# Performance work log

Measured on AMD Instinct MI355X. Metric: run time of the kernel, lower is better.

## Reference

```python
import jax, jax.numpy as jnp
import numpy as np

EPS = 1e-4

def _softmax_kernel(data, projection_matrix, is_query):
    # data: [..., n, d], projection_matrix: [m, d]
    d = data.shape[-1]
    m = projection_matrix.shape[0]
    data_normalizer = 1.0 / (d ** 0.25)
    ratio = 1.0 / (m ** 0.5)
    # [..., n, m]
    data_dash = jnp.einsum('...id,jd->...ij', data_normalizer * data, projection_matrix)
    # ||x||^2 / 2 * normalizer^2, shape [..., n, 1]
    diag_data = (jnp.sum(data * data, axis=-1) * 0.5 * data_normalizer ** 2)[..., None]
    if is_query:
        stab = jnp.max(data_dash, axis=-1, keepdims=True)
    else:
        stab = jnp.max(data_dash)
    return ratio * (jnp.exp(data_dash - diag_data - stab) + EPS)

def _linear_attention(q, k, v):
    # q,k: [..., n, m] feature maps; v: [..., n, e]
    D_inv = 1.0 / jnp.einsum('...nd,...d->...n', q, k.sum(axis=-2))
    context = jnp.einsum('...nd,...ne->...de', k, v)  # [..., m, e]
    return jnp.einsum('...de,...nd,...n->...ne', context, q, D_inv)

def setup_inputs() -> dict:
    key = jax.random.key(0)
    k1, k2, k3, k4 = jax.random.split(key, 4)
    B, H, N, D, M = 8, 8, 4096, 64, 266
    return {
        'q': jax.random.normal(k1, (B, H, N, D), dtype=jnp.float32),
        'k': jax.random.normal(k2, (B, H, N, D), dtype=jnp.float32),
        'v': jax.random.normal(k3, (B, H, N, D), dtype=jnp.float32),
        'projection_matrix': jax.random.normal(k4, (M, D), dtype=jnp.float32),
    }

def reference(q, k, v, projection_matrix):
    q_prime = _softmax_kernel(q, projection_matrix, is_query=True)
    k_prime = _softmax_kernel(k, projection_matrix, is_query=False)
    return _linear_attention(q_prime, k_prime, v)
```

## Files before the change

kernel.cpp:

```cpp
#include <hip/hip_runtime.h>
#include <math.h>

#define BH    64
#define NSEQ  4096
#define DDIM  64
#define MDIM  266
#define MPAD  272
#define CSTR  288
#define KTS   40
#define QTS   296
#define RATIO 0.06131393394849658f
#define NORMF 0.35355339059327373f
#define DIAGF 0.0625f
#define EPSF  1e-4f

typedef __attribute__((ext_vector_type(8))) short bf16x8;
typedef __attribute__((ext_vector_type(4))) float f32x4;

__device__ __forceinline__ unsigned fenc(float f) {
  unsigned u = __float_as_uint(f);
  return (u & 0x80000000u) ? ~u : (u | 0x80000000u);
}
__device__ __forceinline__ float fdec(unsigned u) {
  return (u & 0x80000000u) ? __uint_as_float(u & 0x7fffffffu) : __uint_as_float(~u);
}

__device__ __forceinline__ void split1(float x, unsigned short& h, unsigned short& l) {
  unsigned ux = __float_as_uint(x);
  float hf = __uint_as_float(ux & 0xffff0000u);
  h = (unsigned short)(ux >> 16);
  l = (unsigned short)(__float_as_uint(x - hf) >> 16);
}

__device__ __forceinline__ void splitf(float4 a, float4 b, bf16x8& hi, bf16x8& lo) {
  float x[8] = {a.x, a.y, a.z, a.w, b.x, b.y, b.z, b.w};
#pragma unroll
  for (int e = 0; e < 8; ++e) {
    unsigned short h, l;
    split1(x[e], h, l);
    hi[e] = (short)h;
    lo[e] = (short)l;
  }
}

__device__ __forceinline__ f32x4 mfma3(bf16x8 ah, bf16x8 al, bf16x8 bh, bf16x8 bl, f32x4 acc) {
  acc = __builtin_amdgcn_mfma_f32_16x16x32_bf16(ah, bh, acc, 0, 0, 0);
  acc = __builtin_amdgcn_mfma_f32_16x16x32_bf16(ah, bl, acc, 0, 0, 0);
  acc = __builtin_amdgcn_mfma_f32_16x16x32_bf16(al, bh, acc, 0, 0, 0);
  return acc;
}

__global__ __launch_bounds__(256) void pprep_kernel(const float* __restrict__ proj,
                                                    short* __restrict__ phi,
                                                    short* __restrict__ plo) {
  int idx = blockIdx.x * 256 + threadIdx.x;
  if (idx >= MPAD * DDIM) return;
  int j = idx >> 6;
  float x = (j < MDIM) ? proj[idx] : 0.f;
  unsigned short h, l;
  split1(x, h, l);
  phi[idx] = (short)h;
  plo[idx] = (short)l;
}

__global__ __launch_bounds__(256) void kmax_kernel(const float* __restrict__ k,
                                                   const short* __restrict__ phi,
                                                   const short* __restrict__ plo,
                                                   unsigned* __restrict__ kmax) {
  __shared__ float sK[64 * 76];
  __shared__ float wmax[4];
  const int tid = threadIdx.x;
  const int lane = tid & 63, wv = tid >> 6, lrow = lane & 15, lgrp = lane >> 4;

  float tmax = -1e30f;
  for (int it = 0; it < 8; ++it) {
    const int chunk = blockIdx.x * 8 + it;
    const int bh = chunk >> 6, ch = chunk & 63;
    const float* kb = k + ((size_t)bh * NSEQ + (size_t)ch * 64) * DDIM;
    __syncthreads();
#pragma unroll
    for (int t = 0; t < 4; ++t) {
      int fid = tid + t * 256, r = fid >> 4, d4 = fid & 15;
      *(float4*)&sK[r * 76 + d4 * 4] = ((const float4*)kb)[fid];
    }
    __syncthreads();

    bf16x8 ahi[2], alo[2];
#pragma unroll
    for (int s = 0; s < 2; ++s) {
      const float* p = &sK[(wv * 16 + lrow) * 76 + s * 32 + lgrp * 8];
      splitf(*(const float4*)p, *(const float4*)(p + 4), ahi[s], alo[s]);
    }

#pragma unroll
    for (int jt = 0; jt < 17; ++jt) {
      f32x4 acc = {0.f, 0.f, 0.f, 0.f};
#pragma unroll
      for (int s = 0; s < 2; ++s) {
        const size_t bo = ((size_t)(jt * 16 + lrow)) * DDIM + s * 32 + lgrp * 8;
        acc = mfma3(ahi[s], alo[s], *(const bf16x8*)(phi + bo), *(const bf16x8*)(plo + bo), acc);
      }
      if (jt < 16 || lrow < 10) {
#pragma unroll
        for (int i = 0; i < 4; ++i) tmax = fmaxf(tmax, acc[i]);
      }
    }
  }
#pragma unroll
  for (int off = 32; off; off >>= 1) tmax = fmaxf(tmax, __shfl_xor(tmax, off));
  if (lane == 0) wmax[wv] = tmax;
  __syncthreads();
  if (tid == 0) {
    float m = fmaxf(fmaxf(wmax[0], wmax[1]), fmaxf(wmax[2], wmax[3]));
    atomicMax(kmax, fenc(m * NORMF));
  }
}

__device__ __forceinline__ float dash_reg(int jt, const bf16x8* ahi, const bf16x8* alo,
                                          const bf16x8* ph, const bf16x8* pl,
                                          const float* sDiag, float stab,
                                          unsigned short* kThi, unsigned short* kTlo,
                                          int lrow, int lgrp) {
  float kssum = 0.f;
  const int jg = jt * 16 + lrow;
#pragma unroll
  for (int m = 0; m < 2; ++m) {
    f32x4 d = {0.f, 0.f, 0.f, 0.f};
#pragma unroll
    for (int s = 0; s < 2; ++s)
      d = mfma3(ahi[m * 2 + s], alo[m * 2 + s], ph[s], pl[s], d);
    ushort4 h4, l4;
#pragma unroll
    for (int i = 0; i < 4; ++i) {
      const int nl = m * 16 + lgrp * 4 + i;
      float kd = d[i] * NORMF;
      float kp = (jg < MDIM) ? RATIO * (__expf(kd - sDiag[nl] - stab) + EPSF) : 0.f;
      kssum += kp;
      unsigned short h, l;
      split1(kp, h, l);
      ((unsigned short*)&h4)[i] = h;
      ((unsigned short*)&l4)[i] = l;
    }
    *(ushort4*)&kThi[(size_t)jg * KTS + m * 16 + lgrp * 4] = h4;
    *(ushort4*)&kTlo[(size_t)jg * KTS + m * 16 + lgrp * 4] = l4;
  }
  return kssum;
}

__global__ __launch_bounds__(256, 2) void ctx_kernel(const float* __restrict__ k,
                                                     const float* __restrict__ v,
                                                     const short* __restrict__ phi,
                                                     const short* __restrict__ plo,
                                                     const unsigned* __restrict__ kmaxp,
                                                     float* __restrict__ ctxp,
                                                     float* __restrict__ ksump) {
  __shared__ unsigned short kThi[MPAD * KTS];
  __shared__ unsigned short kTlo[MPAD * KTS];
  __shared__ float sV[32 * 68];
  __shared__ float sDiag[32];
  float* sK = (float*)kThi;

  const int tid = threadIdx.x;
  const int lane = tid & 63, wv = tid >> 6, lrow = lane & 15, lgrp = lane >> 4;
  const int bh = blockIdx.x & 63, c8 = blockIdx.x >> 6;
  const float stab = fdec(*kmaxp);
  const float* kb = k + ((size_t)bh * NSEQ + (size_t)c8 * 512) * DDIM;
  const float* vb = v + ((size_t)bh * NSEQ + (size_t)c8 * 512) * DDIM;

  bf16x8 pfh[4][2], pfl[4][2];
#pragma unroll
  for (int t = 0; t < 4; ++t)
#pragma unroll
    for (int s = 0; s < 2; ++s) {
      const size_t bo = ((size_t)((t * 4 + wv) * 16 + lrow)) * DDIM + s * 32 + lgrp * 8;
      pfh[t][s] = *(const bf16x8*)(phi + bo);
      pfl[t][s] = *(const bf16x8*)(plo + bo);
    }
  bf16x8 pfh4[2], pfl4[2];
  if (wv == 0) {
#pragma unroll
    for (int s = 0; s < 2; ++s) {
      const size_t bo = ((size_t)(256 + lrow)) * DDIM + s * 32 + lgrp * 8;
      pfh4[s] = *(const bf16x8*)(phi + bo);
      pfl4[s] = *(const bf16x8*)(plo + bo);
    }
  }

  f32x4 acc[17];
#pragma unroll
  for (int jt = 0; jt < 17; ++jt) acc[jt] = (f32x4){0.f, 0.f, 0.f, 0.f};
  float ks[5] = {0.f, 0.f, 0.f, 0.f, 0.f};

  for (int rt = 0; rt < 16; ++rt) {
#pragma unroll
    for (int t = 0; t < 2; ++t) {
      int fid = tid + t * 256, r = fid >> 4, d4 = fid & 15;
      *(float4*)&sK[r * 76 + d4 * 4] = ((const float4*)(kb + (size_t)rt * 32 * DDIM))[fid];
      *(float4*)&sV[r * 68 + d4 * 4] = ((const float4*)(vb + (size_t)rt * 32 * DDIM))[fid];
    }
    __syncthreads();
    if (tid < 32) {
      float s = 0.f;
      const float* row = &sK[tid * 76];
#pragma unroll
      for (int d = 0; d < 64; d += 4) {
        float4 x = *(const float4*)(row + d);
        s = fmaf(x.x, x.x, fmaf(x.y, x.y, fmaf(x.z, x.z, fmaf(x.w, x.w, s))));
      }
      sDiag[tid] = s * DIAGF;
    }
    bf16x8 ahi[4], alo[4];
#pragma unroll
    for (int m = 0; m < 2; ++m)
#pragma unroll
      for (int s = 0; s < 2; ++s) {
        const float* p = &sK[(m * 16 + lrow) * 76 + s * 32 + lgrp * 8];
        splitf(*(const float4*)p, *(const float4*)(p + 4), ahi[m * 2 + s], alo[m * 2 + s]);
      }
    bf16x8 vbh, vbl;
    {
      float tv[8];
#pragma unroll
      for (int q = 0; q < 8; ++q) tv[q] = sV[(lgrp * 8 + q) * 68 + wv * 16 + lrow];
      splitf(make_float4(tv[0], tv[1], tv[2], tv[3]),
             make_float4(tv[4], tv[5], tv[6], tv[7]), vbh, vbl);
    }
    __syncthreads();

#pragma unroll
    for (int t = 0; t < 4; ++t)
      ks[t] += dash_reg(t * 4 + wv, ahi, alo, pfh[t], pfl[t], sDiag, stab,
                        kThi, kTlo, lrow, lgrp);
    if (wv == 0)
      ks[4] += dash_reg(16, ahi, alo, pfh4, pfl4, sDiag, stab, kThi, kTlo, lrow, lgrp);
    __syncthreads();

#pragma unroll
    for (int jt = 0; jt < 17; ++jt) {
      bf16x8 ah = *(const bf16x8*)&kThi[(size_t)(jt * 16 + lrow) * KTS + lgrp * 8];
      bf16x8 al = *(const bf16x8*)&kTlo[(size_t)(jt * 16 + lrow) * KTS + lgrp * 8];
      acc[jt] = mfma3(ah, al, vbh, vbl, acc[jt]);
    }
    __syncthreads();
  }

  float* ksb = ksump + (size_t)(c8 * BH + bh) * MPAD;
#pragma unroll
  for (int t = 0; t < 4; ++t) {
    float s = ks[t];
    s += __shfl_xor(s, 16);
    s += __shfl_xor(s, 32);
    if (lgrp == 0) ksb[(t * 4 + wv) * 16 + lrow] = s;
  }
  if (wv == 0) {
    float s = ks[4];
    s += __shfl_xor(s, 16);
    s += __shfl_xor(s, 32);
    if (lgrp == 0) ksb[256 + lrow] = s;
  }
  float* cxb = ctxp + (size_t)(c8 * BH + bh) * MPAD * DDIM;
#pragma unroll
  for (int jt = 0; jt < 17; ++jt)
#pragma unroll
    for (int i = 0; i < 4; ++i)
      cxb[(size_t)(jt * 16 + lgrp * 4 + i) * DDIM + wv * 16 + lrow] = acc[jt][i];
}

__global__ __launch_bounds__(256) void reduce_kernel(const float* __restrict__ ctxp,
                                                     const float* __restrict__ ksump,
                                                     unsigned short* __restrict__ ctxh,
                                                     unsigned short* __restrict__ ctxl,
                                                     float* __restrict__ ksum) {
  const size_t SL = (size_t)BH * MPAD * DDIM;
  const int gid = blockIdx.x * 256 + threadIdx.x;
  if (gid < BH * MPAD * 16) {
    const int e4 = gid & 15;
    const int j = (gid >> 4) % MPAD;
    const int bh = (gid >> 4) / MPAD;
    const size_t base = ((size_t)bh * MPAD + j) * DDIM + e4 * 4;
    float4 s = make_float4(0.f, 0.f, 0.f, 0.f);
#pragma unroll
    for (int c = 0; c < 8; ++c) {
      float4 x = *(const float4*)(ctxp + (size_t)c * SL + base);
      s.x += x.x; s.y += x.y; s.z += x.z; s.w += x.w;
    }
#pragma unroll
    for (int u = 0; u < 4; ++u) {
      unsigned short h, l;
      split1(((const float*)&s)[u], h, l);
      const size_t to = ((size_t)bh * DDIM + e4 * 4 + u) * CSTR + j;
      ctxh[to] = h;
      ctxl[to] = l;
    }
  }
  if (gid < BH * MPAD) {
    float s = 0.f;
#pragma unroll
    for (int c = 0; c < 8; ++c) s += ksump[(size_t)c * BH * MPAD + gid];
    ksum[gid] = s;
  }
}

__global__ __launch_bounds__(256, 2) void out_kernel(const float* __restrict__ q,
                                                     const short* __restrict__ phi,
                                                     const short* __restrict__ plo,
                                                     const unsigned short* __restrict__ ctxh,
                                                     const unsigned short* __restrict__ ctxl,
                                                     const float* __restrict__ ksum,
                                                     float* __restrict__ out) {
  __shared__ unsigned short qThi[32 * QTS];
  __shared__ unsigned short qTlo[32 * QTS];
  __shared__ float sKs[MPAD];
  __shared__ float sDiag[32];
  __shared__ float sMax[128], sSum[128];

  const int tid = threadIdx.x;
  const int lane = tid & 63, wv = tid >> 6, lrow = lane & 15, lgrp = lane >> 4;
  const int bh = blockIdx.x & 63, c16 = blockIdx.x >> 6;
  const float* qb = q + ((size_t)bh * NSEQ + (size_t)c16 * 256) * DDIM;

  for (int t = tid; t < MPAD; t += 256) sKs[t] = ksum[(size_t)bh * MPAD + t];
  for (int idx = tid; idx < 512; idx += 256) {
    const int r = idx >> 4, cc = 272 + (idx & 15);
    qThi[r * QTS + cc] = 0;
    qTlo[r * QTS + cc] = 0;
  }

  bf16x8 cH[9], cL[9];
  {
    const unsigned short* cth = ctxh + ((size_t)bh * DDIM + wv * 16 + lrow) * CSTR;
    const unsigned short* ctl = ctxl + ((size_t)bh * DDIM + wv * 16 + lrow) * CSTR;
#pragma unroll
    for (int kst = 0; kst < 9; ++kst) {
      cH[kst] = *(const bf16x8*)(cth + kst * 32 + lgrp * 8);
      cL[kst] = *(const bf16x8*)(ctl + kst * 32 + lgrp * 8);
    }
  }

  for (int rt = 0; rt < 8; ++rt) {
    bf16x8 qh[4], ql[4];
    float dgp[2];
#pragma unroll
    for (int m = 0; m < 2; ++m) {
      float ss = 0.f;
#pragma unroll
      for (int s = 0; s < 2; ++s) {
        const float* p = qb + (size_t)rt * 32 * DDIM + (m * 16 + lrow) * DDIM + s * 32 + lgrp * 8;
        float4 a = *(const float4*)p;
        float4 b = *(const float4*)(p + 4);
        ss = fmaf(a.x, a.x, fmaf(a.y, a.y, fmaf(a.z, a.z, fmaf(a.w, a.w, ss))));
        ss = fmaf(b.x, b.x, fmaf(b.y, b.y, fmaf(b.z, b.z, fmaf(b.w, b.w, ss))));
        splitf(a, b, qh[m * 2 + s], ql[m * 2 + s]);
      }
      ss += __shfl_xor(ss, 16);
      ss += __shfl_xor(ss, 32);
      dgp[m] = ss * DIAGF;
    }
    if (wv == 0 && lgrp == 0) {
      sDiag[lrow] = dgp[0];
      sDiag[16 + lrow] = dgp[1];
    }

    f32x4 qd[4][2];
#pragma unroll
    for (int t = 0; t < 4; ++t) {
      const size_t bo = ((size_t)((t * 4 + wv) * 16 + lrow)) * DDIM + lgrp * 8;
      bf16x8 ph0 = *(const bf16x8*)(phi + bo);
      bf16x8 pl0 = *(const bf16x8*)(plo + bo);
      bf16x8 ph1 = *(const bf16x8*)(phi + bo + 32);
      bf16x8 pl1 = *(const bf16x8*)(plo + bo + 32);
#pragma unroll
      for (int m = 0; m < 2; ++m) {
        f32x4 d = {0.f, 0.f, 0.f, 0.f};
        d = mfma3(qh[m * 2 + 0], ql[m * 2 + 0], ph0, pl0, d);
        d = mfma3(qh[m * 2 + 1], ql[m * 2 + 1], ph1, pl1, d);
        qd[t][m] = d * NORMF;
      }
    }
    f32x4 qd4[2] = {(f32x4){0.f, 0.f, 0.f, 0.f}, (f32x4){0.f, 0.f, 0.f, 0.f}};
    if (wv == 0) {
      const size_t bo = ((size_t)(256 + lrow)) * DDIM + lgrp * 8;
      bf16x8 ph0 = *(const bf16x8*)(phi + bo);
      bf16x8 pl0 = *(const bf16x8*)(plo + bo);
      bf16x8 ph1 = *(const bf16x8*)(phi + bo + 32);
      bf16x8 pl1 = *(const bf16x8*)(plo + bo + 32);
#pragma unroll
      for (int m = 0; m < 2; ++m) {
        f32x4 d = {0.f, 0.f, 0.f, 0.f};
        d = mfma3(qh[m * 2 + 0], ql[m * 2 + 0], ph0, pl0, d);
        d = mfma3(qh[m * 2 + 1], ql[m * 2 + 1], ph1, pl1, d);
        qd4[m] = d * NORMF;
      }
    }

#pragma unroll
    for (int m = 0; m < 2; ++m)
#pragma unroll
      for (int i = 0; i < 4; ++i) {
        float mx = fmaxf(fmaxf(qd[0][m][i], qd[1][m][i]), fmaxf(qd[2][m][i], qd[3][m][i]));
        if (wv == 0 && lrow < 10) mx = fmaxf(mx, qd4[m][i]);
        mx = fmaxf(mx, __shfl_xor(mx, 1));
        mx = fmaxf(mx, __shfl_xor(mx, 2));
        mx = fmaxf(mx, __shfl_xor(mx, 4));
        mx = fmaxf(mx, __shfl_xor(mx, 8));
        if (lrow == 0) sMax[wv * 32 + m * 16 + lgrp * 4 + i] = mx;
      }
    __syncthreads();

    float mrow[2][4], dgr[2][4], srow[2][4];
#pragma unroll
    for (int m = 0; m < 2; ++m)
#pragma unroll
      for (int i = 0; i < 4; ++i) {
        const int row = m * 16 + lgrp * 4 + i;
        mrow[m][i] = fmaxf(fmaxf(sMax[row], sMax[32 + row]),
                           fmaxf(sMax[64 + row], sMax[96 + row]));
        dgr[m][i] = sDiag[row];
        srow[m][i] = 0.f;
      }
#pragma unroll
    for (int t = 0; t < 4; ++t) {
      const int jg = (t * 4 + wv) * 16 + lrow;
      const float ksj = sKs[jg];
#pragma unroll
      for (int m = 0; m < 2; ++m)
#pragma unroll
        for (int i = 0; i < 4; ++i) {
          float val = RATIO * (__expf(qd[t][m][i] - dgr[m][i] - mrow[m][i]) + EPSF);
          unsigned short h, l;
          split1(val, h, l);
          const int n = m * 16 + lgrp * 4 + i;
          qThi[n * QTS + jg] = h;
          qTlo[n * QTS + jg] = l;
          srow[m][i] = fmaf(val, ksj, srow[m][i]);
        }
    }
    if (wv == 0) {
      const int jg = 256 + lrow;
      const float ksj = sKs[jg];
#pragma unroll
      for (int m = 0; m < 2; ++m)
#pragma unroll
        for (int i = 0; i < 4; ++i) {
          float val = (jg < MDIM) ? RATIO * (__expf(qd4[m][i] - dgr[m][i] - mrow[m][i]) + EPSF)
                                  : 0.f;
          unsigned short h, l;
          split1(val, h, l);
          const int n = m * 16 + lgrp * 4 + i;
          qThi[n * QTS + jg] = h;
          qTlo[n * QTS + jg] = l;
          srow[m][i] = fmaf(val, ksj, srow[m][i]);
        }
    }
#pragma unroll
    for (int m = 0; m < 2; ++m)
#pragma unroll
      for (int i = 0; i < 4; ++i) {
        float s = srow[m][i];
        s += __shfl_xor(s, 1);
        s += __shfl_xor(s, 2);
        s += __shfl_xor(s, 4);
        s += __shfl_xor(s, 8);
        if (lrow == 0) sSum[wv * 32 + m * 16 + lgrp * 4 + i] = s;
      }
    __syncthreads();

    f32x4 acc0 = {0.f, 0.f, 0.f, 0.f}, acc1 = {0.f, 0.f, 0.f, 0.f};
#pragma unroll
    for (int kst = 0; kst < 9; ++kst) {
      bf16x8 ah0 = *(const bf16x8*)&qThi[lrow * QTS + kst * 32 + lgrp * 8];
      bf16x8 al0 = *(const bf16x8*)&qTlo[lrow * QTS + kst * 32 + lgrp * 8];
      acc0 = mfma3(ah0, al0, cH[kst], cL[kst], acc0);
      bf16x8 ah1 = *(const bf16x8*)&qThi[(16 + lrow) * QTS + kst * 32 + lgrp * 8];
      bf16x8 al1 = *(const bf16x8*)&qTlo[(16 + lrow) * QTS + kst * 32 + lgrp * 8];
      acc1 = mfma3(ah1, al1, cH[kst], cL[kst], acc1);
    }
#pragma unroll
    for (int i = 0; i < 4; ++i) {
      const int r0 = lgrp * 4 + i;
      const float d0 = 1.0f / (sSum[r0] + sSum[32 + r0] + sSum[64 + r0] + sSum[96 + r0]);
      out[((size_t)bh * NSEQ + (size_t)c16 * 256 + rt * 32 + r0) * DDIM + wv * 16 + lrow] =
          acc0[i] * d0;
      const int r1 = 16 + lgrp * 4 + i;
      const float d1 = 1.0f / (sSum[r1] + sSum[32 + r1] + sSum[64 + r1] + sSum[96 + r1]);
      out[((size_t)bh * NSEQ + (size_t)c16 * 256 + rt * 32 + r1) * DDIM + wv * 16 + lrow] =
          acc1[i] * d1;
    }
  }
}

extern "C" void kernel_launch(void* const* d_in, const int* in_sizes, int n_in,
                              void* d_out, int out_size, void* d_ws, size_t ws_size,
                              hipStream_t stream) {
  (void)in_sizes; (void)n_in; (void)out_size; (void)ws_size;
  const float* q = (const float*)d_in[0];
  const float* k = (const float*)d_in[1];
  const float* v = (const float*)d_in[2];
  const float* proj = (const float*)d_in[3];
  float* out = (float*)d_out;

  unsigned* kmax = (unsigned*)d_ws;
  unsigned short* ctxh = (unsigned short*)((char*)d_ws + 256);
  unsigned short* ctxl = ctxh + (size_t)BH * DDIM * CSTR;
  float* ksum = (float*)(ctxl + (size_t)BH * DDIM * CSTR);
  short* phi = (short*)(ksum + (size_t)BH * MPAD);
  short* plo = phi + (size_t)MPAD * DDIM;

  const size_t SL = (size_t)BH * MPAD * DDIM;
  float* ctxp = (float*)d_out;
  float* ksump = ctxp + 8 * SL;

  const size_t zb = 256 + 2 * (size_t)BH * DDIM * CSTR * sizeof(unsigned short);
  hipMemsetAsync(d_ws, 0, zb, stream);
  pprep_kernel<<<dim3((MPAD * DDIM + 255) / 256), dim3(256), 0, stream>>>(proj, phi, plo);
  kmax_kernel<<<dim3(512), dim3(256), 0, stream>>>(k, phi, plo, kmax);
  ctx_kernel<<<dim3(BH * 8), dim3(256), 0, stream>>>(k, v, phi, plo, kmax, ctxp, ksump);
  reduce_kernel<<<dim3((BH * MPAD * 16 + 255) / 256), dim3(256), 0, stream>>>(ctxp, ksump,
                                                                              ctxh, ctxl, ksum);
  out_kernel<<<dim3(BH * 16), dim3(256), 0, stream>>>(q, phi, plo, ctxh, ctxl, ksum, out);
}
```

Before: 325.1 us.

## Software-pipeline out_kernel with double-buffered LDS across row tiles

```diff
diff --git a/kernel.cpp b/kernel.cpp
--- a/kernel.cpp
+++ b/kernel.cpp
@@ -308,36 +308,30 @@
                                                      const unsigned short* __restrict__ ctxl,
                                                      const float* __restrict__ ksum,
                                                      float* __restrict__ out) {
-  __shared__ unsigned short qThi[32 * QTS];
-  __shared__ unsigned short qTlo[32 * QTS];
+  __shared__ unsigned short qThi[2][32 * QTS];
+  __shared__ unsigned short qTlo[2][32 * QTS];
   __shared__ float sKs[MPAD];
-  __shared__ float sDiag[32];
-  __shared__ float sMax[128], sSum[128];
+  __shared__ float sDiag[2][32];
+  __shared__ float sMax[2][128], sSum[2][128];
 
   const int tid = threadIdx.x;
   const int lane = tid & 63, wv = tid >> 6, lrow = lane & 15, lgrp = lane >> 4;
   const int bh = blockIdx.x & 63, c16 = blockIdx.x >> 6;
   const float* qb = q + ((size_t)bh * NSEQ + (size_t)c16 * 256) * DDIM;
+  const unsigned short* cth = ctxh + ((size_t)bh * DDIM + wv * 16 + lrow) * CSTR;
+  const unsigned short* ctl = ctxl + ((size_t)bh * DDIM + wv * 16 + lrow) * CSTR;
 
   for (int t = tid; t < MPAD; t += 256) sKs[t] = ksum[(size_t)bh * MPAD + t];
   for (int idx = tid; idx < 512; idx += 256) {
     const int r = idx >> 4, cc = 272 + (idx & 15);
-    qThi[r * QTS + cc] = 0;
-    qTlo[r * QTS + cc] = 0;
-  }
-
-  bf16x8 cH[9], cL[9];
-  {
-    const unsigned short* cth = ctxh + ((size_t)bh * DDIM + wv * 16 + lrow) * CSTR;
-    const unsigned short* ctl = ctxl + ((size_t)bh * DDIM + wv * 16 + lrow) * CSTR;
-#pragma unroll
-    for (int kst = 0; kst < 9; ++kst) {
-      cH[kst] = *(const bf16x8*)(cth + kst * 32 + lgrp * 8);
-      cL[kst] = *(const bf16x8*)(ctl + kst * 32 + lgrp * 8);
-    }
-  }
-
-  for (int rt = 0; rt < 8; ++rt) {
+    qThi[0][r * QTS + cc] = 0; qTlo[0][r * QTS + cc] = 0;
+    qThi[1][r * QTS + cc] = 0; qTlo[1][r * QTS + cc] = 0;
+  }
+
+  f32x4 qd[4][2];
+  f32x4 qd4[2];
+
+  auto dashA = [&](int rt, int p) {
     bf16x8 qh[4], ql[4];
     float dgp[2];
 #pragma unroll
@@ -345,9 +339,9 @@
       float ss = 0.f;
 #pragma unroll
       for (int s = 0; s < 2; ++s) {
-        const float* p = qb + (size_t)rt * 32 * DDIM + (m * 16 + lrow) * DDIM + s * 32 + lgrp * 8;
-        float4 a = *(const float4*)p;
-        float4 b = *(const float4*)(p + 4);
+        const float* pq = qb + (size_t)rt * 32 * DDIM + (m * 16 + lrow) * DDIM + s * 32 + lgrp * 8;
+        float4 a = *(const float4*)pq;
+        float4 b = *(const float4*)(pq + 4);
         ss = fmaf(a.x, a.x, fmaf(a.y, a.y, fmaf(a.z, a.z, fmaf(a.w, a.w, ss))));
         ss = fmaf(b.x, b.x, fmaf(b.y, b.y, fmaf(b.z, b.z, fmaf(b.w, b.w, ss))));
         splitf(a, b, qh[m * 2 + s], ql[m * 2 + s]);
@@ -357,11 +351,9 @@
       dgp[m] = ss * DIAGF;
     }
     if (wv == 0 && lgrp == 0) {
-      sDiag[lrow] = dgp[0];
-      sDiag[16 + lrow] = dgp[1];
-    }
-
-    f32x4 qd[4][2];
+      sDiag[p][lrow] = dgp[0];
+      sDiag[p][16 + lrow] = dgp[1];
+    }
 #pragma unroll
     for (int t = 0; t < 4; ++t) {
       const size_t bo = ((size_t)((t * 4 + wv) * 16 + lrow)) * DDIM + lgrp * 8;
@@ -377,7 +369,8 @@
         qd[t][m] = d * NORMF;
       }
     }
-    f32x4 qd4[2] = {(f32x4){0.f, 0.f, 0.f, 0.f}, (f32x4){0.f, 0.f, 0.f, 0.f}};
+    qd4[0] = (f32x4){0.f, 0.f, 0.f, 0.f};
+    qd4[1] = (f32x4){0.f, 0.f, 0.f, 0.f};
     if (wv == 0) {
       const size_t bo = ((size_t)(256 + lrow)) * DDIM + lgrp * 8;
       bf16x8 ph0 = *(const bf16x8*)(phi + bo);
@@ -392,7 +385,6 @@
         qd4[m] = d * NORMF;
       }
     }
-
 #pragma unroll
     for (int m = 0; m < 2; ++m)
 #pragma unroll
@@ -403,19 +395,20 @@
         mx = fmaxf(mx, __shfl_xor(mx, 2));
         mx = fmaxf(mx, __shfl_xor(mx, 4));
         mx = fmaxf(mx, __shfl_xor(mx, 8));
-        if (lrow == 0) sMax[wv * 32 + m * 16 + lgrp * 4 + i] = mx;
-      }
-    __syncthreads();
-
+        if (lrow == 0) sMax[p][wv * 32 + m * 16 + lgrp * 4 + i] = mx;
+      }
+  };
+
+  auto expB = [&](int p) {
     float mrow[2][4], dgr[2][4], srow[2][4];
 #pragma unroll
     for (int m = 0; m < 2; ++m)
 #pragma unroll
       for (int i = 0; i < 4; ++i) {
         const int row = m * 16 + lgrp * 4 + i;
-        mrow[m][i] = fmaxf(fmaxf(sMax[row], sMax[32 + row]),
-                           fmaxf(sMax[64 + row], sMax[96 + row]));
-        dgr[m][i] = sDiag[row];
+        mrow[m][i] = fmaxf(fmaxf(sMax[p][row], sMax[p][32 + row]),
+                           fmaxf(sMax[p][64 + row], sMax[p][96 + row]));
+        dgr[m][i] = sDiag[p][row];
         srow[m][i] = 0.f;
       }
 #pragma unroll
@@ -430,8 +423,8 @@
           unsigned short h, l;
           split1(val, h, l);
           const int n = m * 16 + lgrp * 4 + i;
-          qThi[n * QTS + jg] = h;
-          qTlo[n * QTS + jg] = l;
+          qThi[p][n * QTS + jg] = h;
+          qTlo[p][n * QTS + jg] = l;
           srow[m][i] = fmaf(val, ksj, srow[m][i]);
         }
     }
@@ -447,8 +440,8 @@
           unsigned short h, l;
           split1(val, h, l);
           const int n = m * 16 + lgrp * 4 + i;
-          qThi[n * QTS + jg] = h;
-          qTlo[n * QTS + jg] = l;
+          qThi[p][n * QTS + jg] = h;
+          qTlo[p][n * QTS + jg] = l;
           srow[m][i] = fmaf(val, ksj, srow[m][i]);
         }
     }
@@ -461,30 +454,53 @@
         s += __shfl_xor(s, 2);
         s += __shfl_xor(s, 4);
         s += __shfl_xor(s, 8);
-        if (lrow == 0) sSum[wv * 32 + m * 16 + lgrp * 4 + i] = s;
-      }
-    __syncthreads();
-
+        if (lrow == 0) sSum[p][wv * 32 + m * 16 + lgrp * 4 + i] = s;
+      }
+  };
+
+  auto gemm2 = [&](int rt, int p) {
+    bf16x8 cH[9], cL[9];
+#pragma unroll
+    for (int kst = 0; kst < 9; ++kst) {
+      cH[kst] = *(const bf16x8*)(cth + kst * 32 + lgrp * 8);
+      cL[kst] = *(const bf16x8*)(ctl + kst * 32 + lgrp * 8);
+    }
     f32x4 acc0 = {0.f, 0.f, 0.f, 0.f}, acc1 = {0.f, 0.f, 0.f, 0.f};
 #pragma unroll
     for (int kst = 0; kst < 9; ++kst) {
-      bf16x8 ah0 = *(const bf16x8*)&qThi[lrow * QTS + kst * 32 + lgrp * 8];
-      bf16x8 al0 = *(const bf16x8*)&qTlo[lrow * QTS + kst * 32 + lgrp * 8];
+      bf16x8 ah0 = *(const bf16x8*)&qThi[p][lrow * QTS + kst * 32 + lgrp * 8];
+      bf16x8 al0 = *(const bf16x8*)&qTlo[p][lrow * QTS + kst * 32 + lgrp * 8];
       acc0 = mfma3(ah0, al0, cH[kst], cL[kst], acc0);
-      bf16x8 ah1 = *(const bf16x8*)&qThi[(16 + lrow) * QTS + kst * 32 + lgrp * 8];
-      bf16x8 al1 = *(const bf16x8*)&qTlo[(16 + lrow) * QTS + kst * 32 + lgrp * 8];
+      bf16x8 ah1 = *(const bf16x8*)&qThi[p][(16 + lrow) * QTS + kst * 32 + lgrp * 8];
+      bf16x8 al1 = *(const bf16x8*)&qTlo[p][(16 + lrow) * QTS + kst * 32 + lgrp * 8];
       acc1 = mfma3(ah1, al1, cH[kst], cL[kst], acc1);
     }
 #pragma unroll
     for (int i = 0; i < 4; ++i) {
       const int r0 = lgrp * 4 + i;
-      const float d0 = 1.0f / (sSum[r0] + sSum[32 + r0] + sSum[64 + r0] + sSum[96 + r0]);
+      const float d0 = 1.0f / (sSum[p][r0] + sSum[p][32 + r0] + sSum[p][64 + r0] + sSum[p][96 + r0]);
       out[((size_t)bh * NSEQ + (size_t)c16 * 256 + rt * 32 + r0) * DDIM + wv * 16 + lrow] =
           acc0[i] * d0;
       const int r1 = 16 + lgrp * 4 + i;
-      const float d1 = 1.0f / (sSum[r1] + sSum[32 + r1] + sSum[64 + r1] + sSum[96 + r1]);
+      const float d1 = 1.0f / (sSum[p][r1] + sSum[p][32 + r1] + sSum[p][64 + r1] + sSum[p][96 + r1]);
       out[((size_t)bh * NSEQ + (size_t)c16 * 256 + rt * 32 + r1) * DDIM + wv * 16 + lrow] =
           acc1[i] * d1;
+    }
+  };
+
+  dashA(0, 0);
+  __syncthreads();
+  expB(0);
+  __syncthreads();
+
+  for (int i = 0; i < 8; ++i) {
+    const int p = i & 1;
+    if (i < 7) dashA(i + 1, p ^ 1);
+    gemm2(i, p);
+    __syncthreads();
+    if (i < 7) {
+      expB(p ^ 1);
+      __syncthreads();
     }
   }
 }
```

Measured after the change: 354.4 us. +9.0%, slower.
